# Kernel tuning notes

Hardware: AMD Instinct MI355X
Metric: run time of the kernel (lower is better)

The kernel has to match this reference:

```python
import jax, jax.numpy as jnp
import numpy as np

D_MODEL, N, L_MAX, BATCH = 512, 64, 2048, 8


def _hippo_pq_lambda(n):
    # HiPPO-LegS matrix -> NPLR decomposition (numpy, done once at setup)
    i = np.arange(n)
    A = np.sqrt(2 * i + 1)[:, None] * np.sqrt(2 * i + 1)[None, :]
    A = np.tril(A, -1) + np.diag(i + 1.0)
    p0 = 0.5 * np.sqrt(2 * np.arange(1, n + 1) - 1.0)
    q0 = 2.0 * p0
    S = -A + p0[:, None] * q0[None, :]
    lam, V = np.linalg.eig(S)
    Vc = V.conj().T
    p = Vc @ p0.astype(np.complex128)
    q = Vc @ q0.astype(np.complex128)
    return lam, p, q


def _c2r(x):
    return np.stack([x.real, x.imag], axis=-1).astype(np.float32)


def setup_inputs() -> dict:
    key = jax.random.key(0)
    ks = jax.random.split(key, 6)
    lam, p, q = _hippo_pq_lambda(N)
    log_step_scale = float(np.log(0.1) - np.log(0.001))
    xavier_std = (2.0 / (D_MODEL + N)) ** 0.5
    return {
        "u": jax.random.normal(ks[0], (BATCH, L_MAX, D_MODEL), jnp.float32),
        "lam": jnp.asarray(_c2r(lam)),            # (N, 2) complex-as-real
        "p": jnp.asarray(_c2r(p)),                # (N, 2)
        "q": jnp.asarray(_c2r(q)),                # (N, 2)
        "B": jax.random.normal(ks[1], (D_MODEL, N, 2), jnp.float32) * xavier_std,
        "Ct": jax.random.normal(ks[2], (D_MODEL, N, 2), jnp.float32) * xavier_std,
        "D": jnp.ones((D_MODEL,), jnp.float32),
        "log_step": jax.random.uniform(ks[3], (D_MODEL,), jnp.float32) * log_step_scale + float(np.log(0.001)),
        "W": jax.random.normal(ks[4], (D_MODEL, D_MODEL), jnp.float32) / (D_MODEL ** 0.5),
        "b": jnp.zeros((D_MODEL,), jnp.float32),
        "gamma": jnp.ones((D_MODEL,), jnp.float32),
        "beta": jnp.zeros((D_MODEL,), jnp.float32),
    }


def _cplx(x):
    return x[..., 0] + 1j * x[..., 1]


def _s4_kernel(lam, p, q, B, Ct, step, l_max):
    # Generating function of the DPLR SSM kernel evaluated at roots of unity,
    # then inverse FFT -> length-l_max convolution kernel K, shape (d_model, l_max).
    omega = jnp.exp(2j * jnp.pi * jnp.arange(l_max) / l_max)  # (L,)
    a0, a1 = jnp.conj(Ct), jnp.conj(q)   # (d,n), (n,)
    b0, b1 = B, p                        # (d,n), (n,)
    v = jnp.stack([
        a0 * b0,
        a0 * b1[None, :],
        a1[None, :] * b0,
        jnp.broadcast_to((a1 * b1)[None, :], B.shape),
    ])  # (4, d, n)
    f = (2.0 / step)[:, None] * ((1.0 - omega) / (1.0 + omega))[None, :]  # (d, L)
    r = 1.0 / (f[:, :, None] - lam)      # (d, L, n)  -- dominant intermediate
    k = jnp.einsum('kdn,dln->kdl', v, r) # 4 Cauchy dots in one contraction
    at_roots = (2.0 / (1.0 + omega)) * (k[0] - k[1] * (1.0 / (1.0 + k[3])) * k[2])
    return jnp.fft.ifft(at_roots, n=l_max, axis=-1).real  # (d, L)


def _s4_block(u, lam, p, q, B, Ct, D, log_step, W, b, gamma, beta):
    L = u.shape[1]
    K = _s4_kernel(_cplx(lam), _cplx(p), _cplx(q), _cplx(B), _cplx(Ct), jnp.exp(log_step), L)
    # non-circular convolution via zero-padded FFT
    ud = jnp.fft.rfft(jnp.pad(u, ((0, 0), (0, L), (0, 0))), axis=1)   # (b, L+1, d)
    Kd = jnp.fft.rfft(jnp.pad(K, ((0, 0), (0, L))), axis=-1)          # (d, L+1)
    y = jnp.fft.irfft(ud * Kd.T[None], axis=1)[:, :L, :] + D * u      # S4Layer out
    y = jax.nn.gelu(y, approximate=False)                             # nn.GELU (exact)
    y = y @ W.T + b                                                   # nn.Linear
    y = y + u                                                         # Residual
    mu = jnp.mean(y, axis=-1, keepdims=True)                          # LayerNorm (post)
    var = jnp.mean((y - mu) ** 2, axis=-1, keepdims=True)
    return (y - mu) * jax.lax.rsqrt(var + 1e-5) * gamma + beta


def reference(u, lam, p, q, B, Ct, D, log_step, W, b, gamma, beta):
    return _s4_block(u, lam, p, q, B, Ct, D, log_step, W, b, gamma, beta)
```

## Files before the change

kernel.cpp:

```cpp
#include <hip/hip_runtime.h>
#include <math.h>

#define DM 512
#define NS 64
#define LS 2048
#define NB 8
#define LF 4096
#define LSP (LS + (LS>>5))

typedef float2 cf;
using bf16x8 = __attribute__((ext_vector_type(8))) short;
using f32x4  = __attribute__((ext_vector_type(4))) float;

__device__ __forceinline__ cf cmul(cf a, cf b){ return make_float2(a.x*b.x - a.y*b.y, a.x*b.y + a.y*b.x); }
__device__ __forceinline__ cf cadd(cf a, cf b){ return make_float2(a.x+b.x, a.y+b.y); }
__device__ __forceinline__ cf csub(cf a, cf b){ return make_float2(a.x-b.x, a.y-b.y); }
__device__ __forceinline__ cf cconjf(cf a){ return make_float2(a.x, -a.y); }
__device__ __forceinline__ cf cscalef(cf a, float s){ return make_float2(a.x*s, a.y*s); }
__device__ __forceinline__ cf cdiv_fast(cf a, cf b){
  float inv = __builtin_amdgcn_rcpf(b.x*b.x + b.y*b.y);
  return make_float2((a.x*b.x + a.y*b.y)*inv, (a.y*b.x - a.x*b.y)*inv);
}

__device__ __forceinline__ float gelu_f(float x){
  return 0.5f*x*(1.0f + erff(x*0.7071067811865475f));
}

__device__ __forceinline__ ushort f2bf(float x){
  uint u = __float_as_uint(x);
  return (ushort)((u + 0x7fffu + ((u>>16)&1u)) >> 16);
}

__device__ __forceinline__ int lp(int x){ return x + (x >> 5); }

__device__ __forceinline__ float2 f2add(float2 a, float2 b){ return make_float2(a.x+b.x, a.y+b.y); }
__device__ __forceinline__ float2 f2mul(float2 a, float2 b){ return make_float2(a.x*b.x, a.y*b.y); }
__device__ __forceinline__ float2 f2fma(float2 a, float2 b, float2 c){
  return make_float2(fmaf(a.x,b.x,c.x), fmaf(a.y,b.y,c.y));
}
__device__ __forceinline__ float2 splat2(float s){ return make_float2(s,s); }
__device__ __forceinline__ float2 rcp2(float2 a){
  return make_float2(__builtin_amdgcn_rcpf(a.x), __builtin_amdgcn_rcpf(a.y));
}

template<int N, int T, bool INV>
__device__ float2* fft_stockham4(float2* a, float2* b, int tid) {
  float2* src = a; float2* dst = b;
  const float base = (INV ? 6.283185307179586f : -6.283185307179586f) / (float)N;
  const float sg = INV ? 1.0f : -1.0f;
  int m = 1;
  while (m * 4 <= N) {
    __syncthreads();
    #pragma unroll
    for (int ii = 0; ii < N/4/T; ii++) {
      int i = tid + ii*T;
      int j = i & ~(m-1);
      float2 c0 = src[i];
      float2 c1 = src[i + N/4];
      float2 c2 = src[i + 2*(N/4)];
      float2 c3 = src[i + 3*(N/4)];
      float2 s02 = cadd(c0,c2), d02 = csub(c0,c2);
      float2 s13 = cadd(c1,c3), d13 = csub(c1,c3);
      float2 jd13 = make_float2(-sg*d13.y, sg*d13.x);
      float2 y0 = cadd(s02, s13);
      float2 y1 = cadd(d02, jd13);
      float2 y2 = csub(s02, s13);
      float2 y3 = csub(d02, jd13);
      float ang = base * (float)j;
      float sn, cs; __sincosf(ang, &sn, &cs);
      float2 w1 = make_float2(cs, sn);
      float2 w2 = cmul(w1, w1);
      float2 w3 = cmul(w2, w1);
      int o = i + 3*j;
      dst[o]       = y0;
      dst[o + m]   = cmul(y1, w1);
      dst[o + 2*m] = cmul(y2, w2);
      dst[o + 3*m] = cmul(y3, w3);
    }
    float2* tswap = src; src = dst; dst = tswap;
    m <<= 2;
  }
  if (m * 2 <= N) {
    __syncthreads();
    #pragma unroll
    for (int ii = 0; ii < N/2/T; ii++) {
      int i = tid + ii*T;
      int j = i & ~(m-1);
      float2 c0 = src[i], c1 = src[i + N/2];
      float ang = base * (float)j;
      float sn, cs; __sincosf(ang, &sn, &cs);
      float2 sum = cadd(c0,c1), dif = csub(c0,c1);
      dst[i + j]     = sum;
      dst[i + j + m] = cmul(dif, make_float2(cs,sn));
    }
    float2* tswap = src; src = dst; dst = tswap;
    m <<= 1;
  }
  __syncthreads();
  return src;
}

template<int N, int T, bool INV>
__device__ float2* fft_stockham8(float2* a, float2* b, int tid) {
  float2* src = a; float2* dst = b;
  const float base = (INV ? 6.283185307179586f : -6.283185307179586f) / (float)N;
  const float sg = INV ? 1.0f : -1.0f;
  const float C8 = 0.70710678118654752f;
  int m = 1;
  while (m * 8 <= N) {
    __syncthreads();
    #pragma unroll
    for (int ii = 0; ii < N/8/T; ii++) {
      int i = tid + ii*T;
      int j = i & ~(m-1);
      float2 c[8];
      #pragma unroll
      for (int t = 0; t < 8; t++) c[t] = src[lp(i + t*(N/8))];
      float2 s0=cadd(c[0],c[4]), d0=csub(c[0],c[4]);
      float2 s1=cadd(c[1],c[5]), d1=csub(c[1],c[5]);
      float2 s2=cadd(c[2],c[6]), d2=csub(c[2],c[6]);
      float2 s3=cadd(c[3],c[7]), d3=csub(c[3],c[7]);
      float2 t1 = make_float2(C8*(d1.x - sg*d1.y), C8*(d1.y + sg*d1.x));
      float2 t2 = make_float2(-sg*d2.y, sg*d2.x);
      float2 t3 = make_float2(-C8*(d3.x + sg*d3.y), C8*(sg*d3.x - d3.y));
      float2 es=cadd(s0,s2), ed=csub(s0,s2), fs=cadd(s1,s3), fd=csub(s1,s3);
      float2 je = make_float2(-sg*fd.y, sg*fd.x);
      float2 y0=cadd(es,fs), y4=csub(es,fs);
      float2 y2=cadd(ed,je), y6=csub(ed,je);
      float2 os=cadd(d0,t2), od=csub(d0,t2), ps=cadd(t1,t3), pd=csub(t1,t3);
      float2 jo = make_float2(-sg*pd.y, sg*pd.x);
      float2 y1=cadd(os,ps), y5=csub(os,ps);
      float2 y3=cadd(od,jo), y7=csub(od,jo);
      float ang = base*(float)j;
      float sn, cs; __sincosf(ang, &sn, &cs);
      float2 w1 = make_float2(cs, sn);
      float2 w2 = cmul(w1,w1), w3 = cmul(w2,w1), w4 = cmul(w2,w2);
      float2 w5 = cmul(w4,w1), w6 = cmul(w4,w2), w7 = cmul(w4,w3);
      int o = i + 7*j;
      dst[lp(o)]       = y0;
      dst[lp(o + m)]   = cmul(y1,w1);
      dst[lp(o + 2*m)] = cmul(y2,w2);
      dst[lp(o + 3*m)] = cmul(y3,w3);
      dst[lp(o + 4*m)] = cmul(y4,w4);
      dst[lp(o + 5*m)] = cmul(y5,w5);
      dst[lp(o + 6*m)] = cmul(y6,w6);
      dst[lp(o + 7*m)] = cmul(y7,w7);
    }
    float2* tswap = src; src = dst; dst = tswap;
    m <<= 3;
  }
  if (m * 4 <= N) {
    __syncthreads();
    #pragma unroll
    for (int ii = 0; ii < N/4/T; ii++) {
      int i = tid + ii*T;
      int j = i & ~(m-1);
      float2 c0 = src[lp(i)];
      float2 c1 = src[lp(i + N/4)];
      float2 c2 = src[lp(i + 2*(N/4))];
      float2 c3 = src[lp(i + 3*(N/4))];
      float2 s02 = cadd(c0,c2), d02 = csub(c0,c2);
      float2 s13 = cadd(c1,c3), d13 = csub(c1,c3);
      float2 jd13 = make_float2(-sg*d13.y, sg*d13.x);
      float2 y0 = cadd(s02, s13);
      float2 y1 = cadd(d02, jd13);
      float2 y2 = csub(s02, s13);
      float2 y3 = csub(d02, jd13);
      float ang = base * (float)j;
      float sn, cs; __sincosf(ang, &sn, &cs);
      float2 w1 = make_float2(cs, sn);
      float2 w2 = cmul(w1, w1);
      float2 w3 = cmul(w2, w1);
      int o = i + 3*j;
      dst[lp(o)]       = y0;
      dst[lp(o + m)]   = cmul(y1, w1);
      dst[lp(o + 2*m)] = cmul(y2, w2);
      dst[lp(o + 3*m)] = cmul(y3, w3);
    }
    float2* tswap = src; src = dst; dst = tswap;
    m <<= 2;
  }
  if (m * 2 <= N) {
    __syncthreads();
    #pragma unroll
    for (int ii = 0; ii < N/2/T; ii++) {
      int i = tid + ii*T;
      int j = i & ~(m-1);
      float2 c0 = src[lp(i)], c1 = src[lp(i + N/2)];
      float ang = base * (float)j;
      float sn, cs; __sincosf(ang, &sn, &cs);
      float2 sum = cadd(c0,c1), dif = csub(c0,c1);
      dst[lp(i + j)]     = sum;
      dst[lp(i + j + m)] = cmul(dif, make_float2(cs,sn));
    }
    float2* tswap = src; src = dst; dst = tswap;
    m <<= 1;
  }
  __syncthreads();
  return src;
}


__device__ void transpose_body(const float* __restrict__ u, float* __restrict__ ut,
                               int idx, int tid, float* tileRaw)
{
  float (*tile)[33] = reinterpret_cast<float(*)[33]>(tileRaw);
  int t0 = (idx & 63) * 32;
  int d0 = ((idx >> 6) & 15) * 32;
  int b  = idx >> 10;
  int tx = tid & 31;
  int ty = tid >> 5;
  #pragma unroll
  for (int r = 0; r < 32; r += 8)
    tile[ty + r][tx] = u[((size_t)b*LS + t0 + ty + r)*DM + d0 + tx];
  __syncthreads();
  #pragma unroll
  for (int r = 0; r < 32; r += 8)
    ut[((size_t)b*DM + d0 + ty + r)*LS + t0 + tx] = tile[tx][ty + r];
}

__device__ void cauchy_body(const float* __restrict__ lam_g, const float* __restrict__ p_g,
                            const float* __restrict__ q_g,   const float* __restrict__ B_g,
                            const float* __restrict__ Ct_g,  const float* __restrict__ logstep_g,
                            float2* __restrict__ at, int idx, int tid, float* tabRaw)
{
  float (*tab)[12] = reinterpret_cast<float(*)[12]>(tabRaw);
  int d     = idx & 511;
  int chunk = idx >> 9;
  float tos = 2.0f / expf(logstep_g[d]);
  float invtos = __builtin_amdgcn_rcpf(tos);

  if (tid < NS) {
    int n = tid;
    float lx = lam_g[2*n], ly = lam_g[2*n+1];
    cf pn   = make_float2(p_g[2*n],   p_g[2*n+1]);
    cf qn   = make_float2(q_g[2*n],   q_g[2*n+1]);
    cf Bdn  = make_float2(B_g[(d*NS+n)*2],  B_g[(d*NS+n)*2+1]);
    cf Cdn  = make_float2(Ct_g[(d*NS+n)*2], Ct_g[(d*NS+n)*2+1]);
    cf a0 = cconjf(Cdn);
    cf a1 = cconjf(qn);
    cf w0 = cmul(a0, Bdn);
    cf w1 = cmul(a0, pn);
    cf w2 = cmul(a1, Bdn);
    cf w3 = cmul(a1, pn);
    tab[n][0] = -lx;  tab[n][1] = ly;   tab[n][2] = lx*lx; tab[n][3] = w0.x;
    tab[n][4] = w0.y; tab[n][5] = w1.x; tab[n][6] = w1.y;  tab[n][7] = w2.x;
    tab[n][8] = w2.y; tab[n][9] = w3.x; tab[n][10] = w3.y; tab[n][11] = 0.f;
  }

  float2 g2[2];
  #pragma unroll
  for (int sp = 0; sp < 2; sp++) {
    float gg[2];
    #pragma unroll
    for (int h = 0; h < 2; h++) {
      int l = chunk*1024 + (2*sp + h)*256 + tid;
      float half_ang = 3.14159265358979323846f * (float)l / (float)LS;
      float sn, cs;
      sincosf(half_ang, &sn, &cs);
      gg[h] = tos * (sn / cs);
    }
    g2[sp] = make_float2(gg[0], gg[1]);
  }
  __syncthreads();

  float2 k0x[2], k0y[2], k1x[2], k1y[2], k2x[2], k2y[2], k3x[2], k3y[2];
  #pragma unroll
  for (int sp = 0; sp < 2; sp++) {
    k0x[sp] = splat2(0.f); k0y[sp] = splat2(0.f);
    k1x[sp] = splat2(0.f); k1y[sp] = splat2(0.f);
    k2x[sp] = splat2(0.f); k2y[sp] = splat2(0.f);
    k3x[sp] = splat2(0.f); k3y[sp] = splat2(0.f);
  }

  #pragma unroll 2
  for (int n = 0; n < NS; n++) {
    float4 t0 = *reinterpret_cast<const float4*>(&tab[n][0]);
    float4 t1 = *reinterpret_cast<const float4*>(&tab[n][4]);
    float4 t2 = *reinterpret_cast<const float4*>(&tab[n][8]);
    #pragma unroll
    for (int sp = 0; sp < 2; sp++) {
      float2 e   = f2add(g2[sp], splat2(t0.y));
      float2 mag = f2fma(e, e, splat2(t0.z));
      float2 inv = rcp2(mag);
      float2 rx  = f2mul(splat2(t0.x), inv);
      float2 ry  = f2mul(e, inv);
      k0x[sp] = f2fma(splat2(t0.w), rx, k0x[sp]);
      k0x[sp] = f2fma(splat2(-t1.x), ry, k0x[sp]);
      k0y[sp] = f2fma(splat2(t0.w), ry, k0y[sp]);
      k0y[sp] = f2fma(splat2(t1.x), rx, k0y[sp]);
      k1x[sp] = f2fma(splat2(t1.y), rx, k1x[sp]);
      k1x[sp] = f2fma(splat2(-t1.z), ry, k1x[sp]);
      k1y[sp] = f2fma(splat2(t1.y), ry, k1y[sp]);
      k1y[sp] = f2fma(splat2(t1.z), rx, k1y[sp]);
      k2x[sp] = f2fma(splat2(t1.w), rx, k2x[sp]);
      k2x[sp] = f2fma(splat2(-t2.x), ry, k2x[sp]);
      k2y[sp] = f2fma(splat2(t1.w), ry, k2y[sp]);
      k2y[sp] = f2fma(splat2(t2.x), rx, k2y[sp]);
      k3x[sp] = f2fma(splat2(t2.y), rx, k3x[sp]);
      k3x[sp] = f2fma(splat2(-t2.z), ry, k3x[sp]);
      k3y[sp] = f2fma(splat2(t2.y), ry, k3y[sp]);
      k3y[sp] = f2fma(splat2(t2.z), rx, k3y[sp]);
    }
  }

  #pragma unroll
  for (int sp = 0; sp < 2; sp++) {
    #pragma unroll
    for (int h = 0; h < 2; h++) {
      int l = chunk*1024 + (2*sp + h)*256 + tid;
      float gv = (h == 0) ? g2[sp].x : g2[sp].y;
      cf k0 = make_float2(h==0?k0x[sp].x:k0x[sp].y, h==0?k0y[sp].x:k0y[sp].y);
      cf k1 = make_float2(h==0?k1x[sp].x:k1x[sp].y, h==0?k1y[sp].x:k1y[sp].y);
      cf k2 = make_float2(h==0?k2x[sp].x:k2x[sp].y, h==0?k2y[sp].x:k2y[sp].y);
      cf k3 = make_float2(h==0?k3x[sp].x:k3x[sp].y, h==0?k3y[sp].x:k3y[sp].y);
      cf t1c = cdiv_fast(cmul(k1, k2), make_float2(1.0f + k3.x, k3.y));
      cf inner = csub(k0, t1c);
      cf c2 = make_float2(1.0f, -gv * invtos);
      at[(size_t)d*LS + l] = cmul(c2, inner);
    }
  }
}

__device__ void wb_body(const float* __restrict__ W, ushort* __restrict__ Wb,
                        int idx, int tid)
{
  int i = (idx*256 + tid)*4;
  float4 v = *reinterpret_cast<const float4*>(W + i);
  uint2 o;
  o.x = (uint)f2bf(v.x) | ((uint)f2bf(v.y) << 16);
  o.y = (uint)f2bf(v.z) | ((uint)f2bf(v.w) << 16);
  *reinterpret_cast<uint2*>(Wb + i) = o;
}

__global__ __launch_bounds__(256) void fused0_kernel(
    const float* __restrict__ u, float* __restrict__ ut,
    const float* __restrict__ lam_g, const float* __restrict__ p_g,
    const float* __restrict__ q_g,   const float* __restrict__ B_g,
    const float* __restrict__ Ct_g,  const float* __restrict__ logstep_g,
    float2* __restrict__ at,
    const float* __restrict__ W, ushort* __restrict__ Wb)
{
  __shared__ float lds[32*33];
  int bid = blockIdx.x;
  int tid = threadIdx.x;
  if (bid < 9216) {
    int g = bid / 9, r = bid % 9;
    if (r < 8) transpose_body(u, ut, g*8 + r, tid, lds);
    else       cauchy_body(lam_g, p_g, q_g, B_g, Ct_g, logstep_g, at, g, tid, lds);
  } else {
    wb_body(W, Wb, bid - 9216, tid);
  }
}

__global__ __launch_bounds__(256) void kfft_kernel(
    const float2* __restrict__ at, float2* __restrict__ Kf)
{
  __shared__ float2 bufA[LSP];
  __shared__ float2 bufB[LSP];
  int tid = threadIdx.x;
  int d0 = blockIdx.x * 2;
  const float2* at0 = at + (size_t)d0*LS;
  const float2* at1 = at0 + LS;
  float2* Kf0 = Kf + (size_t)d0*LF;
  float2* Kf1 = Kf0 + LF;

  #pragma unroll
  for (int s = 0; s < 8; s++) {
    int k = tid + s*256;
    int nk = (LS - k) & (LS - 1);
    cf a0k = at0[k], a0n = at0[nk];
    cf a1k = at1[k], a1n = at1[nk];
    cf H0 = make_float2(0.5f*(a0k.x + a0n.x), 0.5f*(a0k.y - a0n.y));
    cf H1 = make_float2(0.5f*(a1k.x + a1n.x), 0.5f*(a1k.y - a1n.y));
    Kf0[k] = H0;
    Kf1[k] = H1;
    bufA[lp(k)] = make_float2(H0.x - H1.y, H0.y + H1.x);
  }
  float2* res = fft_stockham8<LS, 256, true>(bufA, bufB, tid);
  float2* other = (res == bufA) ? bufB : bufA;
  #pragma unroll
  for (int s = 0; s < 8; s++) {
    int t = tid + s*256;
    float ang = 3.14159265358979323846f * (float)t / (float)LS;
    float sn, cs;
    __sincosf(ang, &sn, &cs);
    cf Kc = cscalef(res[lp(t)], 1.0f/(float)LS);
    other[lp(t)] = cmul(Kc, make_float2(cs, -sn));
  }
  float2* G = fft_stockham8<LS, 256, false>(other, res, tid);
  #pragma unroll
  for (int s = 0; s < 4; s++) {
    int k = tid + s*256;
    int rk = LS - 1 - k;
    cf Gk = G[lp(k)], Gr = G[lp(rk)];
    cf F0 = make_float2(0.5f*(Gk.x + Gr.x), 0.5f*(Gk.y - Gr.y));
    cf F1 = make_float2(0.5f*(Gk.y + Gr.y), 0.5f*(Gr.x - Gk.x));
    Kf0[LS + k]  = F0;
    Kf0[LS + rk] = cconjf(F0);
    Kf1[LS + k]  = F1;
    Kf1[LS + rk] = cconjf(F1);
  }
}

__global__ __launch_bounds__(512) void conv_kernel(
    const float* __restrict__ ut, const float2* __restrict__ Kf,
    const float* __restrict__ Dv, ushort* __restrict__ gb)
{
  __shared__ float2 bufA[LS];
  __shared__ float2 bufB[LS];
  int tid = threadIdx.x;
  int d0 = blockIdx.x * 2;
  int b  = blockIdx.y;
  const float* u0p = ut + ((size_t)b*DM + d0)*LS;
  const float* u1p = u0p + LS;
  const float2* Kf0 = Kf + (size_t)d0 * LF;
  const float2* Kf1 = Kf0 + LF;
  float u0r[4], u1r[4];
  #pragma unroll
  for (int s = 0; s < 4; s++) {
    int t = tid + s*512;
    u0r[s] = u0p[t]; u1r[s] = u1p[t];
    bufA[t] = make_float2(u0r[s], u1r[s]);
  }

  float2* Z  = fft_stockham4<LS, 512, false>(bufA, bufB, tid);
  float2* Wb = (Z == bufA) ? bufB : bufA;
  #pragma unroll
  for (int s = 0; s < 4; s++) {
    int mq = tid + s*512;
    int mm = (LS - mq) & (LS - 1);
    cf Za = Z[mq], Zb = Z[mm];
    cf U0 = make_float2(0.5f*(Za.x + Zb.x), 0.5f*(Za.y - Zb.y));
    cf U1 = make_float2(0.5f*(Za.y + Zb.y), 0.5f*(Zb.x - Za.x));
    cf Y0 = cmul(U0, Kf0[mq]);
    cf Y1 = cmul(U1, Kf1[mq]);
    Wb[mq] = make_float2(Y0.x - Y1.y, Y0.y + Y1.x);
  }
  float2* A = fft_stockham4<LS, 512, true>(Wb, Z, tid);
  float2 areg[4];
  #pragma unroll
  for (int s = 0; s < 4; s++) areg[s] = A[tid + s*512];

  float2* st = (A == bufA) ? bufB : bufA;
  #pragma unroll
  for (int s = 0; s < 4; s++) {
    int t = tid + s*512;
    float ang = -3.14159265358979323846f * (float)t / (float)LS;
    float sn, cs; __sincosf(ang, &sn, &cs);
    cf z = make_float2(u0r[s], u1r[s]);
    st[t] = cmul(z, make_float2(cs, sn));
  }
  float2* Z2  = fft_stockham4<LS, 512, false>(st, A, tid);
  float2* Wb2 = (Z2 == bufA) ? bufB : bufA;
  #pragma unroll
  for (int s = 0; s < 4; s++) {
    int mq = tid + s*512;
    int mm = LS - 1 - mq;
    cf Za = Z2[mq], Zb = Z2[mm];
    cf U0 = make_float2(0.5f*(Za.x + Zb.x), 0.5f*(Za.y - Zb.y));
    cf U1 = make_float2(0.5f*(Za.y + Zb.y), 0.5f*(Zb.x - Za.x));
    cf Y0 = cmul(U0, Kf0[LS + mq]);
    cf Y1 = cmul(U1, Kf1[LS + mq]);
    Wb2[mq] = make_float2(Y0.x - Y1.y, Y0.y + Y1.x);
  }
  float2* C = fft_stockham4<LS, 512, true>(Wb2, Z2, tid);

  float dv0 = Dv[d0], dv1 = Dv[d0+1];
  ushort* g0 = gb + ((size_t)b*DM + d0)*LS;
  ushort* g1 = g0 + LS;
  #pragma unroll
  for (int s = 0; s < 4; s++) {
    int t = tid + s*512;
    float ang = 3.14159265358979323846f * (float)t / (float)LS;
    float sn, cs; __sincosf(ang, &sn, &cs);
    cf c = C[t];
    cf bb = cmul(c, make_float2(cs, sn));
    float y0 = (areg[s].x + bb.x) * (1.0f/LF) + dv0 * u0r[s];
    float y1 = (areg[s].y + bb.y) * (1.0f/LF) + dv1 * u1r[s];
    g0[t] = f2bf(gelu_f(y0));
    g1[t] = f2bf(gelu_f(y1));
  }
}

__global__ __launch_bounds__(256) void transposeT_kernel(
    const ushort* __restrict__ gb, ushort* __restrict__ gt)
{
  __shared__ ushort tile[64][65];
  int b  = blockIdx.z;
  int t0 = blockIdx.x * 64;
  int d0 = blockIdx.y * 64;
  int tx = threadIdx.x & 31;
  int ty = threadIdx.x >> 5;
  #pragma unroll
  for (int r = 0; r < 8; r++) {
    int d = ty + r*8;
    uint v = *reinterpret_cast<const uint*>(&gb[((size_t)b*DM + d0 + d)*LS + t0 + tx*2]);
    tile[d][tx*2]   = (ushort)(v & 0xffffu);
    tile[d][tx*2+1] = (ushort)(v >> 16);
  }
  __syncthreads();
  #pragma unroll
  for (int r = 0; r < 8; r++) {
    int t = ty + r*8;
    uint lo = tile[tx*2][t];
    uint hi = tile[tx*2+1][t];
    *reinterpret_cast<uint*>(&gt[((size_t)b*LS + t0 + t)*DM + d0 + tx*2]) = lo | (hi << 16);
  }
}

__global__ __launch_bounds__(512) void gemm_ln_kernel(
    const ushort* __restrict__ gt, const ushort* __restrict__ Wbm,
    const float* __restrict__ bias, const float* __restrict__ u,
    const float* __restrict__ gamma, const float* __restrict__ beta,
    float* __restrict__ out)
{
  __shared__ ushort As[64*64];
  __shared__ ushort Bs[512*64];
  __shared__ float red[2][64][4];
  int tid = threadIdx.x;
  int b  = blockIdx.y;
  int t0 = blockIdx.x * 64;
  int wid = tid >> 6, lane = tid & 63;
  int wm = wid >> 2, wn = wid & 3;
  int m = lane & 15, q = lane >> 4;

  f32x4 acc[2][8];
  #pragma unroll
  for (int i = 0; i < 2; i++)
    #pragma unroll
    for (int j = 0; j < 8; j++)
      acc[i][j] = (f32x4){0.f, 0.f, 0.f, 0.f};

  const ushort* Ag = gt + ((size_t)b*LS + t0)*DM;

  for (int k0 = 0; k0 < DM; k0 += 64) {
    {
      int r = tid >> 3, g = tid & 7;
      uint4 va = *reinterpret_cast<const uint4*>(Ag + (size_t)r*DM + k0 + g*8);
      *reinterpret_cast<uint4*>(&As[r*64 + ((g ^ (r&7))*8)]) = va;
    }
    #pragma unroll
    for (int i = 0; i < 8; i++) {
      int idx = tid + i*512;
      int r = idx >> 3, g = idx & 7;
      uint4 vb = *reinterpret_cast<const uint4*>(Wbm + (size_t)r*DM + k0 + g*8);
      *reinterpret_cast<uint4*>(&Bs[r*64 + ((g ^ (r&7))*8)]) = vb;
    }
    __syncthreads();
    #pragma unroll
    for (int kk = 0; kk < 64; kk += 32) {
      int gk = (kk >> 3) + q;
      bf16x8 af[2], bfr[8];
      #pragma unroll
      for (int mi = 0; mi < 2; mi++) {
        int row = wm*32 + mi*16 + m;
        af[mi] = *reinterpret_cast<const bf16x8*>(&As[row*64 + ((gk ^ (row&7))*8)]);
      }
      #pragma unroll
      for (int ni = 0; ni < 8; ni++) {
        int row = wn*128 + ni*16 + m;
        bfr[ni] = *reinterpret_cast<const bf16x8*>(&Bs[row*64 + ((gk ^ (row&7))*8)]);
      }
      #pragma unroll
      for (int mi = 0; mi < 2; mi++)
        #pragma unroll
        for (int ni = 0; ni < 8; ni++)
          acc[mi][ni] = __builtin_amdgcn_mfma_f32_16x16x32_bf16(af[mi], bfr[ni], acc[mi][ni], 0, 0, 0);
    }
    __syncthreads();
  }

  float sum_[2][4], sq_[2][4];
  #pragma unroll
  for (int mi = 0; mi < 2; mi++)
    #pragma unroll
    for (int jj = 0; jj < 4; jj++) { sum_[mi][jj] = 0.f; sq_[mi][jj] = 0.f; }

  #pragma unroll
  for (int mi = 0; mi < 2; mi++) {
    #pragma unroll
    for (int ni = 0; ni < 8; ni++) {
      int col = wn*128 + ni*16 + m;
      float bb = bias[col];
      #pragma unroll
      for (int jj = 0; jj < 4; jj++) {
        int row = t0 + wm*32 + mi*16 + q*4 + jj;
        float y = acc[mi][ni][jj] + bb + u[((size_t)b*LS + row)*DM + col];
        acc[mi][ni][jj] = y;
        sum_[mi][jj] += y;
        sq_[mi][jj]  += y*y;
      }
    }
  }
  #pragma unroll
  for (int mi = 0; mi < 2; mi++)
    #pragma unroll
    for (int jj = 0; jj < 4; jj++) {
      #pragma unroll
      for (int off = 1; off < 16; off <<= 1) {
        sum_[mi][jj] += __shfl_xor(sum_[mi][jj], off, 64);
        sq_[mi][jj]  += __shfl_xor(sq_[mi][jj],  off, 64);
      }
    }
  if (m == 0) {
    #pragma unroll
    for (int mi = 0; mi < 2; mi++)
      #pragma unroll
      for (int jj = 0; jj < 4; jj++) {
        int rowl = wm*32 + mi*16 + q*4 + jj;
        red[0][rowl][wn] = sum_[mi][jj];
        red[1][rowl][wn] = sq_[mi][jj];
      }
  }
  __syncthreads();
  #pragma unroll
  for (int mi = 0; mi < 2; mi++) {
    #pragma unroll
    for (int jj = 0; jj < 4; jj++) {
      int rowl = wm*32 + mi*16 + q*4 + jj;
      float s  = red[0][rowl][0] + red[0][rowl][1] + red[0][rowl][2] + red[0][rowl][3];
      float s2 = red[1][rowl][0] + red[1][rowl][1] + red[1][rowl][2] + red[1][rowl][3];
      float mu  = s * (1.0f/DM);
      float var = s2 * (1.0f/DM) - mu*mu;
      float rs  = rsqrtf(var + 1e-5f);
      int row = t0 + rowl;
      #pragma unroll
      for (int ni = 0; ni < 8; ni++) {
        int col = wn*128 + ni*16 + m;
        size_t off = ((size_t)b*LS + row)*DM + col;
        out[off] = (acc[mi][ni][jj] - mu) * rs * gamma[col] + beta[col];
      }
    }
  }
}

extern "C" void kernel_launch(void* const* d_in, const int* in_sizes, int n_in,
                              void* d_out, int out_size, void* d_ws, size_t ws_size,
                              hipStream_t stream) {
  const float* u       = (const float*)d_in[0];
  const float* lam     = (const float*)d_in[1];
  const float* p       = (const float*)d_in[2];
  const float* q       = (const float*)d_in[3];
  const float* B       = (const float*)d_in[4];
  const float* Ct      = (const float*)d_in[5];
  const float* Dv      = (const float*)d_in[6];
  const float* logstep = (const float*)d_in[7];
  const float* W       = (const float*)d_in[8];
  const float* bias    = (const float*)d_in[9];
  const float* gamma   = (const float*)d_in[10];
  const float* beta    = (const float*)d_in[11];
  float* out = (float*)d_out;

  char* wsb = (char*)d_ws;
  float2* Kf  = (float2*)wsb;
  ushort* gt  = (ushort*)wsb;
  ushort* gb  = (ushort*)(wsb + (size_t)16*1024*1024);
  float2* at  = (float2*)(wsb + (size_t)32*1024*1024);
  ushort* Wbm = (ushort*)(wsb + (size_t)40*1024*1024);
  float* ut = (float*)d_out;

  fused0_kernel<<<dim3(9472), 256, 0, stream>>>(u, ut, lam, p, q, B, Ct, logstep, at, W, Wbm);
  kfft_kernel<<<dim3(DM/2), 256, 0, stream>>>(at, Kf);
  conv_kernel<<<dim3(DM/2, NB), 512, 0, stream>>>(ut, Kf, Dv, gb);
  transposeT_kernel<<<dim3(LS/64, DM/64, NB), 256, 0, stream>>>(gb, gt);
  gemm_ln_kernel<<<dim3(LS/64, NB), 512, 0, stream>>>(gt, Wbm, bias, u, gamma, beta, out);
}
```

Measured before the change: 154.9 us.

## Fuse transpose into GEMM by loading activations d-major and transposing in LDS

Removes the separate transpose kernel and its global round trip. The GEMM now reads the conv output directly in (d, t) layout, stores it into a padded LDS tile, and gathers A fragments with strided scalar LDS reads. This saves memory traffic and one launch, but adds more LDS read instructions and possible bank conflicts in the MFMA inner loop.

```diff
diff --git a/kernel.cpp b/kernel.cpp
--- a/kernel.cpp
+++ b/kernel.cpp
@@ -483,39 +483,14 @@
   }
 }
 
-__global__ __launch_bounds__(256) void transposeT_kernel(
-    const ushort* __restrict__ gb, ushort* __restrict__ gt)
-{
-  __shared__ ushort tile[64][65];
-  int b  = blockIdx.z;
-  int t0 = blockIdx.x * 64;
-  int d0 = blockIdx.y * 64;
-  int tx = threadIdx.x & 31;
-  int ty = threadIdx.x >> 5;
-  #pragma unroll
-  for (int r = 0; r < 8; r++) {
-    int d = ty + r*8;
-    uint v = *reinterpret_cast<const uint*>(&gb[((size_t)b*DM + d0 + d)*LS + t0 + tx*2]);
-    tile[d][tx*2]   = (ushort)(v & 0xffffu);
-    tile[d][tx*2+1] = (ushort)(v >> 16);
-  }
-  __syncthreads();
-  #pragma unroll
-  for (int r = 0; r < 8; r++) {
-    int t = ty + r*8;
-    uint lo = tile[tx*2][t];
-    uint hi = tile[tx*2+1][t];
-    *reinterpret_cast<uint*>(&gt[((size_t)b*LS + t0 + t)*DM + d0 + tx*2]) = lo | (hi << 16);
-  }
-}
-
+#define ASTRIDE 68
 __global__ __launch_bounds__(512) void gemm_ln_kernel(
-    const ushort* __restrict__ gt, const ushort* __restrict__ Wbm,
+    const ushort* __restrict__ gb, const ushort* __restrict__ Wbm,
     const float* __restrict__ bias, const float* __restrict__ u,
     const float* __restrict__ gamma, const float* __restrict__ beta,
     float* __restrict__ out)
 {
-  __shared__ ushort As[64*64];
+  __shared__ ushort Ast[64*ASTRIDE];
   __shared__ ushort Bs[512*64];
   __shared__ float red[2][64][4];
   int tid = threadIdx.x;
@@ -532,13 +507,12 @@
     for (int j = 0; j < 8; j++)
       acc[i][j] = (f32x4){0.f, 0.f, 0.f, 0.f};
 
-  const ushort* Ag = gt + ((size_t)b*LS + t0)*DM;
-
   for (int k0 = 0; k0 < DM; k0 += 64) {
     {
       int r = tid >> 3, g = tid & 7;
-      uint4 va = *reinterpret_cast<const uint4*>(Ag + (size_t)r*DM + k0 + g*8);
-      *reinterpret_cast<uint4*>(&As[r*64 + ((g ^ (r&7))*8)]) = va;
+      uint4 va = *reinterpret_cast<const uint4*>(gb + ((size_t)b*DM + k0 + r)*LS + t0 + g*8);
+      *reinterpret_cast<uint2*>(&Ast[r*ASTRIDE + g*8])     = make_uint2(va.x, va.y);
+      *reinterpret_cast<uint2*>(&Ast[r*ASTRIDE + g*8 + 4]) = make_uint2(va.z, va.w);
     }
     #pragma unroll
     for (int i = 0; i < 8; i++) {
@@ -554,8 +528,12 @@
       bf16x8 af[2], bfr[8];
       #pragma unroll
       for (int mi = 0; mi < 2; mi++) {
-        int row = wm*32 + mi*16 + m;
-        af[mi] = *reinterpret_cast<const bf16x8*>(&As[row*64 + ((gk ^ (row&7))*8)]);
+        int trow = wm*32 + mi*16 + m;
+        bf16x8 v;
+        #pragma unroll
+        for (int e = 0; e < 8; e++)
+          v[e] = (short)Ast[(gk*8 + e)*ASTRIDE + trow];
+        af[mi] = v;
       }
       #pragma unroll
       for (int ni = 0; ni < 8; ni++) {
@@ -654,7 +632,6 @@
 
   char* wsb = (char*)d_ws;
   float2* Kf  = (float2*)wsb;
-  ushort* gt  = (ushort*)wsb;
   ushort* gb  = (ushort*)(wsb + (size_t)16*1024*1024);
   float2* at  = (float2*)(wsb + (size_t)32*1024*1024);
   ushort* Wbm = (ushort*)(wsb + (size_t)40*1024*1024);
@@ -663,6 +640,5 @@
   fused0_kernel<<<dim3(9472), 256, 0, stream>>>(u, ut, lam, p, q, B, Ct, logstep, at, W, Wbm);
   kfft_kernel<<<dim3(DM/2), 256, 0, stream>>>(at, Kf);
   conv_kernel<<<dim3(DM/2, NB), 512, 0, stream>>>(ut, Kf, Dv, gb);
-  transposeT_kernel<<<dim3(LS/64, DM/64, NB), 256, 0, stream>>>(gb, gt);
-  gemm_ln_kernel<<<dim3(LS/64, NB), 512, 0, stream>>>(gt, Wbm, bias, u, gamma, beta, out);
-}
+  gemm_ln_kernel<<<dim3(LS/64, NB), 512, 0, stream>>>(gb, Wbm, bias, u, gamma, beta, out);
+}
```

Measured after the change: 145.7 us. 1.06x faster.
